# Performance work log

Measured on AMD Instinct MI355X. Metric: run time of the kernel, lower is better.

Reference implementation:

```python
import jax, jax.numpy as jnp
import numpy as np

EPS_MSG = 1e-7   # GENConv message eps
EPS_LN = 1e-5    # LayerNorm eps

N, F_IN, D, D_OUT = 32768, 64, 512, 128


def setup_inputs() -> dict:
    key = jax.random.key(0)
    ks = jax.random.split(key, 20)
    s = 0.02
    inp = {
        "batch": jax.random.normal(ks[0], (1, N, F_IN), jnp.float32),
        "W_enc": jax.random.normal(ks[1], (F_IN, D), jnp.float32) * s,
        "b_enc": jnp.zeros((D,), jnp.float32),
        "Wf": jax.random.normal(ks[2], (D, D_OUT), jnp.float32) * s,
        "bf": jnp.zeros((D_OUT,), jnp.float32),
    }
    for l in range(2):
        inp[f"t{l}"] = jnp.array(1.0, jnp.float32)           # learnable softmax temperature
        inp[f"W1_{l}"] = jax.random.normal(ks[3 + 6 * l], (D, 2 * D), jnp.float32) * s
        inp[f"b1_{l}"] = jnp.zeros((2 * D,), jnp.float32)
        inp[f"g_{l}"] = jnp.ones((2 * D,), jnp.float32)      # LN gamma
        inp[f"be_{l}"] = jnp.zeros((2 * D,), jnp.float32)    # LN beta
        inp[f"W2_{l}"] = jax.random.normal(ks[4 + 6 * l], (2 * D, D), jnp.float32) * s
        inp[f"b2_{l}"] = jnp.zeros((D,), jnp.float32)
    return inp


def _layer_norm(z, g, b):
    mu = jnp.mean(z, axis=-1, keepdims=True)
    var = jnp.var(z, axis=-1, keepdims=True)
    return (z - mu) * jax.lax.rsqrt(var + EPS_LN) * g + b


def _deepgcn_layer(x, t, W1, b1, g, be, W2, b2):
    # res+ block: h = conv(act(norm(x))); return x + h   (norm is Identity here)
    h = jax.nn.relu(x)                       # [n, d]
    # GENConv with complete graph: msg_j = relu(h_j) + eps (independent of target i)
    m = jax.nn.relu(h) + EPS_MSG             # [n, d]
    alpha = jax.nn.softmax(t * m, axis=0)    # per-channel softmax over all source nodes
    agg = jnp.sum(alpha * m, axis=0)         # [d]  -- identical for every target node
    out = h + agg[None, :]                   # + x_dst residual inside GENConv
    # GENConv MLP: Linear(d,2d) -> LayerNorm -> ReLU -> Linear(2d,d)
    z = jax.nn.relu(_layer_norm(out @ W1 + b1, g, be))
    out = z @ W2 + b2
    return x + out


def reference(batch, W_enc, b_enc, Wf, bf,
              t0, W1_0, b1_0, g_0, be_0, W2_0, b2_0,
              t1, W1_1, b1_1, g_1, be_1, W2_1, b2_1):
    bsz, n, _ = batch.shape
    x = batch.reshape(bsz * n, -1) @ W_enc + b_enc   # node encoder
    x = _deepgcn_layer(x, t0, W1_0, b1_0, g_0, be_0, W2_0, b2_0)
    x = _deepgcn_layer(x, t1, W1_1, b1_1, g_1, be_1, W2_1, b2_1)
    x = jax.nn.relu(x)                               # layers[0].act(layers[0].norm(x)), norm=Identity
    out = x @ Wf + bf
    return out.reshape(bsz, n, -1)
```

## Files before the change

kernel.cpp:

```cpp
#include <hip/hip_runtime.h>

#define DEV __device__ __forceinline__

typedef __attribute__((ext_vector_type(8))) short s8v;
typedef __attribute__((ext_vector_type(4))) float f4v;

DEV short f2bf(float f) {
  unsigned u = __builtin_bit_cast(unsigned, f);
  u += 0x7fffu + ((u >> 16) & 1u);
  return (short)(u >> 16);
}
DEV float bf2f(short s) {
  unsigned u = ((unsigned)(unsigned short)s) << 16;
  return __builtin_bit_cast(float, u);
}

DEV f4v mfma_16x16x32_bf16(s8v a, s8v b, f4v c) {
  asm("v_mfma_f32_16x16x32_bf16 %0, %1, %2, %0" : "+v"(c) : "v"(a), "v"(b));
  return c;
}

__global__ __launch_bounds__(256) void tconv_k(const float* __restrict__ in,
                                               short* __restrict__ out,
                                               int K, int N) {
  __shared__ float t[64][65];
  const int nb = blockIdx.x * 64, kb = blockIdx.y * 64;
  const int c = threadIdx.x & 63, r0 = threadIdx.x >> 6;
#pragma unroll
  for (int rr = 0; rr < 64; rr += 4)
    t[rr + r0][c] = in[(size_t)(kb + rr + r0) * N + nb + c];
  __syncthreads();
#pragma unroll
  for (int rr = 0; rr < 64; rr += 4)
    out[(size_t)(nb + rr + r0) * K + kb + c] = f2bf(t[c][rr + r0]);
}

__global__ __launch_bounds__(256) void conv_k(const float* __restrict__ in,
                                              short* __restrict__ out, int n4) {
  int i = blockIdx.x * 256 + threadIdx.x;
  if (i >= n4) return;
  float4 v = ((const float4*)in)[i];
  short4 o;
  o.x = f2bf(v.x);
  o.y = f2bf(v.y);
  o.z = f2bf(v.z);
  o.w = f2bf(v.w);
  ((short4*)out)[i] = o;
}

__global__ __launch_bounds__(256) void zero_k(float* p, int n) {
  int i = blockIdx.x * 256 + threadIdx.x;
  if (i < n) p[i] = 0.f;
}

__global__ __launch_bounds__(256) void finalize_k(const float* __restrict__ sums,
                                                  const float* __restrict__ W1,
                                                  const float* __restrict__ b1,
                                                  float* __restrict__ biasEff) {
  __shared__ float agg[512];
  const int tid = threadIdx.x;
  for (int d = tid; d < 512; d += 256) agg[d] = sums[512 + d] / sums[d];
  __syncthreads();
  const int j = blockIdx.x * 256 + tid;
  float a = b1[j];
  for (int d = 0; d < 512; ++d) a += agg[d] * W1[(size_t)d * 1024 + j];
  biasEff[j] = a;
}

__global__ __launch_bounds__(256) void ln_relu_k(short* __restrict__ z,
                                                 const float* __restrict__ g,
                                                 const float* __restrict__ be) {
  const int row = blockIdx.x * 4 + (threadIdx.x >> 6);
  const int lane = threadIdx.x & 63;
  short* zr = z + (size_t)row * 1024;
  s8v c0 = *(const s8v*)&zr[lane * 8];
  s8v c1 = *(const s8v*)&zr[512 + lane * 8];
  float v[16];
  float s = 0.f, q = 0.f;
#pragma unroll
  for (int i = 0; i < 8; ++i) { v[i] = bf2f(c0[i]); v[8 + i] = bf2f(c1[i]); }
#pragma unroll
  for (int i = 0; i < 16; ++i) { s += v[i]; q += v[i] * v[i]; }
#pragma unroll
  for (int o = 32; o > 0; o >>= 1) { s += __shfl_xor(s, o); q += __shfl_xor(q, o); }
  float mu = s * (1.f / 1024.f);
  float var = q * (1.f / 1024.f) - mu * mu;
  float rs = rsqrtf(var + 1e-5f);
  float gv[16], bv[16];
#pragma unroll
  for (int i = 0; i < 8; ++i) {
    gv[i] = g[lane * 8 + i];      gv[8 + i] = g[512 + lane * 8 + i];
    bv[i] = be[lane * 8 + i];     bv[8 + i] = be[512 + lane * 8 + i];
  }
  s8v o0, o1;
#pragma unroll
  for (int i = 0; i < 8; ++i) {
    o0[i] = f2bf(fmaxf((v[i] - mu) * rs * gv[i] + bv[i], 0.f));
    o1[i] = f2bf(fmaxf((v[8 + i] - mu) * rs * gv[8 + i] + bv[8 + i], 0.f));
  }
  *(s8v*)&zr[lane * 8] = o0;
  *(s8v*)&zr[512 + lane * 8] = o1;
}

#define F_ADD  1
#define F_WF32 2
#define F_WBF  4
#define F_WH   8
#define F_SM   16

template <int FLAGS>
__global__ __launch_bounds__(256) void gemm_k(const short* __restrict__ A,
                                              const short* __restrict__ Bt,
                                              const float* __restrict__ bias,
                                              const float* __restrict__ Xin,
                                              float* __restrict__ Xout,
                                              short* __restrict__ Cb,
                                              const float* __restrict__ tptr,
                                              float* __restrict__ sums,
                                              int M, int N, int K) {
  __shared__ short lA[128 * 32];
  __shared__ short lB[128 * 32];
  const int tid = threadIdx.x;
  const int lane = tid & 63, wid = tid >> 6;
  const int wr = wid >> 1, wc = wid & 1;
  const int nwg = gridDim.x * gridDim.y;
  const int wg = blockIdx.y * gridDim.x + blockIdx.x;
  const int swz = (wg & 7) * (nwg >> 3) + (wg >> 3);
  const int bx = swz % gridDim.x, by = swz / gridDim.x;
  const int brow = by * 128, bcol = bx * 128;
  const int l15 = lane & 15, lhi = lane >> 4;
  f4v acc[4][4] = {};

  for (int k0 = 0; k0 < K; k0 += 32) {
#pragma unroll
    for (int r = 0; r < 2; ++r) {
      int chunk = r * 256 + wid * 64 + lane;
      int row = chunk >> 2, kc = (chunk & 3) << 3;
      const short* ga = A + (size_t)(brow + row) * K + (k0 + kc);
      const short* gb = Bt + (size_t)(bcol + row) * K + (k0 + kc);
      __builtin_amdgcn_global_load_lds(
          (const __attribute__((address_space(1))) void*)ga,
          (__attribute__((address_space(3))) void*)&lA[(r * 256 + wid * 64) * 8],
          16, 0, 0);
      __builtin_amdgcn_global_load_lds(
          (const __attribute__((address_space(1))) void*)gb,
          (__attribute__((address_space(3))) void*)&lB[(r * 256 + wid * 64) * 8],
          16, 0, 0);
    }
    __syncthreads();
    s8v af[4], bfr[4];
#pragma unroll
    for (int i = 0; i < 4; ++i) {
      af[i]  = *(const s8v*)&lA[(wr * 64 + i * 16 + l15) * 32 + lhi * 8];
      bfr[i] = *(const s8v*)&lB[(wc * 64 + i * 16 + l15) * 32 + lhi * 8];
    }
#pragma unroll
    for (int mi = 0; mi < 4; ++mi)
#pragma unroll
      for (int ni = 0; ni < 4; ++ni)
        acc[mi][ni] = mfma_16x16x32_bf16(af[mi], bfr[ni], acc[mi][ni]);
    __syncthreads();
  }

  const float tv = (FLAGS & F_SM) ? tptr[0] : 0.f;
  float* sred = (float*)lA;
  if (FLAGS & F_SM) {
    sred[tid] = 0.f;
    __syncthreads();
  }
#pragma unroll
  for (int ni = 0; ni < 4; ++ni) {
    int col = bcol + wc * 64 + ni * 16 + l15;
    float bv = bias[col];
    float se = 0.f, sem = 0.f;
#pragma unroll
    for (int mi = 0; mi < 4; ++mi) {
#pragma unroll
      for (int r = 0; r < 4; ++r) {
        int row = brow + wr * 64 + mi * 16 + lhi * 4 + r;
        size_t idx = (size_t)row * N + col;
        float v = acc[mi][ni][r] + bv;
        if (FLAGS & F_ADD) v += Xin[idx];
        if (FLAGS & F_WF32) Xout[idx] = v;
        if (FLAGS & F_WBF) Cb[idx] = f2bf(v);
        if (FLAGS & F_WH) {
          float hh = fmaxf(v, 0.f);
          Cb[idx] = f2bf(hh);
          if (FLAGS & F_SM) {
            float m = hh + 1e-7f;
            float e = __expf(tv * m);
            se += e;
            sem += e * m;
          }
        }
      }
    }
    if (FLAGS & F_SM) {
      se += __shfl_xor(se, 16);  se += __shfl_xor(se, 32);
      sem += __shfl_xor(sem, 16); sem += __shfl_xor(sem, 32);
      if (lhi == 0) {
        atomicAdd(&sred[wc * 64 + ni * 16 + l15], se);
        atomicAdd(&sred[128 + wc * 64 + ni * 16 + l15], sem);
      }
    }
  }
  if (FLAGS & F_SM) {
    __syncthreads();
    int v = tid >> 7, c = tid & 127;
    atomicAdd(&sums[v * 512 + bcol + c], sred[v * 128 + c]);
  }
}

extern "C" void kernel_launch(void* const* d_in, const int* in_sizes, int n_in,
                              void* d_out, int out_size, void* d_ws,
                              size_t ws_size, hipStream_t stream) {
  (void)in_sizes; (void)n_in; (void)out_size; (void)ws_size;
  const float* batch = (const float*)d_in[0];
  const float* W_enc = (const float*)d_in[1];
  const float* b_enc = (const float*)d_in[2];
  const float* Wf    = (const float*)d_in[3];
  const float* bfv   = (const float*)d_in[4];
  const float* tptr[2] = {(const float*)d_in[5],  (const float*)d_in[12]};
  const float* W1[2]   = {(const float*)d_in[6],  (const float*)d_in[13]};
  const float* b1[2]   = {(const float*)d_in[7],  (const float*)d_in[14]};
  const float* g[2]    = {(const float*)d_in[8],  (const float*)d_in[15]};
  const float* be[2]   = {(const float*)d_in[9],  (const float*)d_in[16]};
  const float* W2[2]   = {(const float*)d_in[10], (const float*)d_in[17]};
  const float* b2[2]   = {(const float*)d_in[11], (const float*)d_in[18]};
  float* out = (float*)d_out;

  const int M = 32768;
  char* ws = (char*)d_ws;
  size_t off = 0;
  auto alloc = [&](size_t bytes) -> char* {
    char* p = ws + off;
    off += (bytes + 255) & ~(size_t)255;
    return p;
  };
  float* xf32   = (float*)alloc((size_t)M * 512 * 4);
  short* abuf   = (short*)alloc((size_t)M * 512 * 2);
  short* zbuf   = (short*)alloc((size_t)M * 1024 * 2);
  short* bbuf   = (short*)alloc((size_t)M * 64 * 2);
  short* wencT  = (short*)alloc(512 * 64 * 2);
  short* w1T0   = (short*)alloc(1024 * 512 * 2);
  short* w2T0   = (short*)alloc(512 * 1024 * 2);
  short* w1T1   = (short*)alloc(1024 * 512 * 2);
  short* w2T1   = (short*)alloc(512 * 1024 * 2);
  short* wfT    = (short*)alloc(128 * 512 * 2);
  float* sums   = (float*)alloc(2 * 1024 * 4);
  float* biasEff= (float*)alloc(1024 * 4);
  short* w1T[2] = {w1T0, w1T1};
  short* w2T[2] = {w2T0, w2T1};

  tconv_k<<<dim3(512 / 64, 64 / 64), 256, 0, stream>>>(W_enc, wencT, 64, 512);
  tconv_k<<<dim3(1024 / 64, 512 / 64), 256, 0, stream>>>(W1[0], w1T[0], 512, 1024);
  tconv_k<<<dim3(512 / 64, 1024 / 64), 256, 0, stream>>>(W2[0], w2T[0], 1024, 512);
  tconv_k<<<dim3(1024 / 64, 512 / 64), 256, 0, stream>>>(W1[1], w1T[1], 512, 1024);
  tconv_k<<<dim3(512 / 64, 1024 / 64), 256, 0, stream>>>(W2[1], w2T[1], 1024, 512);
  tconv_k<<<dim3(128 / 64, 512 / 64), 256, 0, stream>>>(Wf, wfT, 512, 128);

  conv_k<<<(M * 64 / 4 + 255) / 256, 256, 0, stream>>>(batch, bbuf, M * 64 / 4);
  zero_k<<<(2048 + 255) / 256, 256, 0, stream>>>(sums, 2048);

  gemm_k<F_WF32 | F_WH | F_SM>
      <<<dim3(512 / 128, M / 128), 256, 0, stream>>>(
          bbuf, wencT, b_enc, nullptr, xf32, abuf, tptr[0], sums, M, 512, 64);

  for (int l = 0; l < 2; ++l) {
    finalize_k<<<4, 256, 0, stream>>>(sums + l * 1024, W1[l], b1[l], biasEff);
    gemm_k<F_WBF><<<dim3(1024 / 128, M / 128), 256, 0, stream>>>(
        abuf, w1T[l], biasEff, nullptr, nullptr, zbuf, nullptr, nullptr,
        M, 1024, 512);
    ln_relu_k<<<M / 4, 256, 0, stream>>>(zbuf, g[l], be[l]);
    if (l == 0) {
      gemm_k<F_ADD | F_WF32 | F_WH | F_SM>
          <<<dim3(512 / 128, M / 128), 256, 0, stream>>>(
              zbuf, w2T[l], b2[l], xf32, xf32, abuf, tptr[1], sums + 1024,
              M, 512, 1024);
    } else {
      gemm_k<F_ADD | F_WH><<<dim3(512 / 128, M / 128), 256, 0, stream>>>(
          zbuf, w2T[l], b2[l], xf32, nullptr, abuf, nullptr, nullptr,
          M, 512, 1024);
    }
  }

  gemm_k<F_WF32><<<dim3(128 / 128, M / 128), 256, 0, stream>>>(
      abuf, wfT, bfv, nullptr, out, nullptr, nullptr, nullptr, M, 128, 512);
}
```

Measured before the change: 456.8 us.

## Keep residual stream in bf16 and apply ReLU on A-fragments in GEMMs

Replaces the separate fp32 residual buffer and the bf16 relu'd activation buffer with a single bf16 residual buffer. ReLU moves into the consuming GEMMs, which apply it to A fragments after the LDS read, and the residual add reads bf16. This cuts epilogue global traffic (no fp32 read/write of the 32768x512 residual, one buffer write instead of two). The cost is lower precision in the residual accumulation across layers and extra per-fragment ALU work in the main loop.

```diff
diff --git a/kernel.cpp b/kernel.cpp
--- a/kernel.cpp
+++ b/kernel.cpp
@@ -18,6 +18,12 @@
 DEV f4v mfma_16x16x32_bf16(s8v a, s8v b, f4v c) {
   asm("v_mfma_f32_16x16x32_bf16 %0, %1, %2, %0" : "+v"(c) : "v"(a), "v"(b));
   return c;
+}
+
+DEV s8v relu8(s8v a) {
+#pragma unroll
+  for (int i = 0; i < 8; ++i) a[i] = a[i] > (short)0 ? a[i] : (short)0;
+  return a;
 }
 
 __global__ __launch_bounds__(256) void tconv_k(const float* __restrict__ in,
@@ -102,19 +108,19 @@
   *(s8v*)&zr[512 + lane * 8] = o1;
 }
 
-#define F_ADD  1
-#define F_WF32 2
-#define F_WBF  4
-#define F_WH   8
-#define F_SM   16
+#define F_ADD   1
+#define F_WF32  2
+#define F_WBF   4
+#define F_SM    8
+#define F_RELUA 16
 
 template <int FLAGS>
 __global__ __launch_bounds__(256) void gemm_k(const short* __restrict__ A,
                                               const short* __restrict__ Bt,
                                               const float* __restrict__ bias,
-                                              const float* __restrict__ Xin,
-                                              float* __restrict__ Xout,
+                                              const short* __restrict__ Xin,
                                               short* __restrict__ Cb,
+                                              float* __restrict__ Cf,
                                               const float* __restrict__ tptr,
                                               float* __restrict__ sums,
                                               int M, int N, int K) {
@@ -153,6 +159,7 @@
     for (int i = 0; i < 4; ++i) {
       af[i]  = *(const s8v*)&lA[(wr * 64 + i * 16 + l15) * 32 + lhi * 8];
       bfr[i] = *(const s8v*)&lB[(wc * 64 + i * 16 + l15) * 32 + lhi * 8];
+      if (FLAGS & F_RELUA) af[i] = relu8(af[i]);
     }
 #pragma unroll
     for (int mi = 0; mi < 4; ++mi)
@@ -180,23 +187,19 @@
         int row = brow + wr * 64 + mi * 16 + lhi * 4 + r;
         size_t idx = (size_t)row * N + col;
         float v = acc[mi][ni][r] + bv;
-        if (FLAGS & F_ADD) v += Xin[idx];
-        if (FLAGS & F_WF32) Xout[idx] = v;
+        if (FLAGS & F_ADD) v += bf2f(Xin[idx]);
+        if (FLAGS & F_WF32) Cf[idx] = v;
         if (FLAGS & F_WBF) Cb[idx] = f2bf(v);
-        if (FLAGS & F_WH) {
-          float hh = fmaxf(v, 0.f);
-          Cb[idx] = f2bf(hh);
-          if (FLAGS & F_SM) {
-            float m = hh + 1e-7f;
-            float e = __expf(tv * m);
-            se += e;
-            sem += e * m;
-          }
+        if (FLAGS & F_SM) {
+          float m = fmaxf(v, 0.f) + 1e-7f;
+          float e = __expf(tv * m);
+          se += e;
+          sem += e * m;
         }
       }
     }
     if (FLAGS & F_SM) {
-      se += __shfl_xor(se, 16);  se += __shfl_xor(se, 32);
+      se += __shfl_xor(se, 16);   se += __shfl_xor(se, 32);
       sem += __shfl_xor(sem, 16); sem += __shfl_xor(sem, 32);
       if (lhi == 0) {
         atomicAdd(&sred[wc * 64 + ni * 16 + l15], se);
@@ -237,8 +240,7 @@
     off += (bytes + 255) & ~(size_t)255;
     return p;
   };
-  float* xf32   = (float*)alloc((size_t)M * 512 * 4);
-  short* abuf   = (short*)alloc((size_t)M * 512 * 2);
+  short* xbf    = (short*)alloc((size_t)M * 512 * 2);
   short* zbuf   = (short*)alloc((size_t)M * 1024 * 2);
   short* bbuf   = (short*)alloc((size_t)M * 64 * 2);
   short* wencT  = (short*)alloc(512 * 64 * 2);
@@ -262,28 +264,26 @@
   conv_k<<<(M * 64 / 4 + 255) / 256, 256, 0, stream>>>(batch, bbuf, M * 64 / 4);
   zero_k<<<(2048 + 255) / 256, 256, 0, stream>>>(sums, 2048);
 
-  gemm_k<F_WF32 | F_WH | F_SM>
-      <<<dim3(512 / 128, M / 128), 256, 0, stream>>>(
-          bbuf, wencT, b_enc, nullptr, xf32, abuf, tptr[0], sums, M, 512, 64);
+  gemm_k<F_WBF | F_SM><<<dim3(512 / 128, M / 128), 256, 0, stream>>>(
+      bbuf, wencT, b_enc, nullptr, xbf, nullptr, tptr[0], sums, M, 512, 64);
 
   for (int l = 0; l < 2; ++l) {
     finalize_k<<<4, 256, 0, stream>>>(sums + l * 1024, W1[l], b1[l], biasEff);
-    gemm_k<F_WBF><<<dim3(1024 / 128, M / 128), 256, 0, stream>>>(
-        abuf, w1T[l], biasEff, nullptr, nullptr, zbuf, nullptr, nullptr,
+    gemm_k<F_WBF | F_RELUA><<<dim3(1024 / 128, M / 128), 256, 0, stream>>>(
+        xbf, w1T[l], biasEff, nullptr, zbuf, nullptr, nullptr, nullptr,
         M, 1024, 512);
     ln_relu_k<<<M / 4, 256, 0, stream>>>(zbuf, g[l], be[l]);
     if (l == 0) {
-      gemm_k<F_ADD | F_WF32 | F_WH | F_SM>
-          <<<dim3(512 / 128, M / 128), 256, 0, stream>>>(
-              zbuf, w2T[l], b2[l], xf32, xf32, abuf, tptr[1], sums + 1024,
-              M, 512, 1024);
+      gemm_k<F_ADD | F_WBF | F_SM><<<dim3(512 / 128, M / 128), 256, 0, stream>>>(
+          zbuf, w2T[l], b2[l], xbf, xbf, nullptr, tptr[1], sums + 1024,
+          M, 512, 1024);
     } else {
-      gemm_k<F_ADD | F_WH><<<dim3(512 / 128, M / 128), 256, 0, stream>>>(
-          zbuf, w2T[l], b2[l], xf32, nullptr, abuf, nullptr, nullptr,
+      gemm_k<F_ADD | F_WBF><<<dim3(512 / 128, M / 128), 256, 0, stream>>>(
+          zbuf, w2T[l], b2[l], xbf, xbf, nullptr, nullptr, nullptr,
           M, 512, 1024);
     }
   }
 
-  gemm_k<F_WF32><<<dim3(128 / 128, M / 128), 256, 0, stream>>>(
-      abuf, wfT, bfv, nullptr, out, nullptr, nullptr, nullptr, M, 128, 512);
-}
+  gemm_k<F_WF32 | F_RELUA><<<dim3(128 / 128, M / 128), 256, 0, stream>>>(
+      xbf, wfT, bfv, nullptr, nullptr, out, nullptr, nullptr, M, 128, 512);
+}
```

After: 426.7 us. 6.6% less time.
